# Kernel tuning notes

Measured on AMD Instinct MI355X. Metric: run time of the kernel, lower is better.

## Reference

```python
import jax, jax.numpy as jnp
import numpy as np

H = 8          # query heads
KVH = 1        # key/value heads
HD = 256       # head dim
ROPE_BASE = 10000.0


def _rotate_half(x):
    x1, x2 = x[..., : HD // 2], x[..., HD // 2 :]
    return jnp.concatenate((-x2, x1), axis=-1)


def _rope_cos_sin(position_ids):
    # position_ids: [B, S] int -> cos/sin: [B, S, HD]
    inv_freq = 1.0 / (ROPE_BASE ** (jnp.arange(0, HD, 2, dtype=jnp.float32) / HD))
    freqs = position_ids.astype(jnp.float32)[..., None] * inv_freq  # [B,S,HD/2]
    emb = jnp.concatenate((freqs, freqs), axis=-1)                  # [B,S,HD]
    return jnp.cos(emb), jnp.sin(emb)


def setup_inputs() -> dict:
    key = jax.random.key(0)
    ks = jax.random.split(key, 5)
    B, S, D = 2, 2048, 2048
    return {
        "hidden_states": jax.random.normal(ks[0], (B, S, D), dtype=jnp.float32),
        "attention_mask": jnp.zeros((B, 1, S, S), dtype=jnp.float32),
        "position_ids": jnp.broadcast_to(jnp.arange(S, dtype=jnp.int32), (B, S)),
        "Wq": jax.random.normal(ks[1], (D, H * HD), dtype=jnp.float32) * 0.02,
        "Wk": jax.random.normal(ks[2], (D, KVH * HD), dtype=jnp.float32) * 0.02,
        "Wv": jax.random.normal(ks[3], (D, KVH * HD), dtype=jnp.float32) * 0.02,
        "Wo": jax.random.normal(ks[4], (H * HD, D), dtype=jnp.float32) * 0.02,
    }


def reference(hidden_states, attention_mask, position_ids, Wq, Wk, Wv, Wo):
    B, S, D = hidden_states.shape
    # projections -> [B, heads, S, HD]
    q = jnp.einsum("bsd,df->bsf", hidden_states, Wq).reshape(B, S, H, HD).transpose(0, 2, 1, 3)
    k = jnp.einsum("bsd,df->bsf", hidden_states, Wk).reshape(B, S, KVH, HD).transpose(0, 2, 1, 3)
    v = jnp.einsum("bsd,df->bsf", hidden_states, Wv).reshape(B, S, KVH, HD).transpose(0, 2, 1, 3)

    cos, sin = _rope_cos_sin(position_ids)
    cos, sin = cos[:, None], sin[:, None]  # unsqueeze head dim
    q = q * cos + _rotate_half(q) * sin
    k = k * cos + _rotate_half(k) * sin

    # GQA: repeat kv heads to match query heads
    rep = H // KVH
    k = jnp.repeat(k, rep, axis=1)
    v = jnp.repeat(v, rep, axis=1)

    d_k = D // H  # matches torch code's scaling (== HD here)
    scores = jnp.einsum("bhqd,bhkd->bhqk", q, k) / jnp.sqrt(jnp.float32(d_k))
    scores = scores + attention_mask
    attn = jax.nn.softmax(scores, axis=-1)  # dropout p=0 / eval mode

    out = jnp.einsum("bhqk,bhkd->bhqd", attn, v)  # [B,H,S,HD]
    out = out.transpose(0, 2, 1, 3).reshape(B, S, H * HD)
    out = jnp.einsum("bsf,fd->bsd", out, Wo)
    return out
```

## Files before the change

### kernel.cpp

```cpp
#include <hip/hip_runtime.h>
#include <cmath>


typedef __bf16 bf16;
typedef __attribute__((ext_vector_type(8))) __bf16 bf16x8;
typedef __attribute__((ext_vector_type(4))) __bf16 bf16x4;
typedef __attribute__((ext_vector_type(4))) float f32x4;

#define S_LEN 2048
#define D_MODEL 2048
#define H_NUM 8
#define HDIM 256
#define NT (S_LEN / 64)
#define SM_BIAS 8.0f

#define BAR __builtin_amdgcn_s_barrier()

__device__ __forceinline__ void gl_lds16(const bf16* g, bf16* l) {
  __builtin_amdgcn_global_load_lds(
      (const __attribute__((address_space(1))) void*)g,
      (__attribute__((address_space(3))) void*)l, 16, 0, 0);
}

__global__ void cvt_bf16(const float* __restrict__ src, bf16* __restrict__ dst) {
  const int i = (blockIdx.x * 256 + threadIdx.x) * 4;
  const float4 v = *(const float4*)(src + i);
  bf16x4 o;
  o[0] = (bf16)v.x; o[1] = (bf16)v.y; o[2] = (bf16)v.z; o[3] = (bf16)v.w;
  *(bf16x4*)(dst + i) = o;
}

__global__ void tpose_all(const float* __restrict__ Wq, const float* __restrict__ Wk,
                          const float* __restrict__ Wv, const float* __restrict__ Wo,
                          bf16* __restrict__ Wqkvt, bf16* __restrict__ Wot) {
  __shared__ float t[32][33];
  const int tx = threadIdx.x, ty = threadIdx.y;
  const int bx = blockIdx.x;
  const int k0 = blockIdx.y * 32;
  const float* W; bf16* Wt; int Ncols, no0, n0;
  if (bx < 64)      { W = Wq; Wt = Wqkvt; Ncols = 2048; no0 = 0;    n0 = bx * 32; }
  else if (bx < 72) { W = Wk; Wt = Wqkvt; Ncols = 256;  no0 = 2048; n0 = (bx - 64) * 32; }
  else if (bx < 80) { W = Wv; Wt = Wqkvt; Ncols = 256;  no0 = 2304; n0 = (bx - 72) * 32; }
  else              { W = Wo; Wt = Wot;   Ncols = 2048; no0 = 0;    n0 = (bx - 80) * 32; }
#pragma unroll
  for (int i = 0; i < 4; ++i)
    t[ty + 8 * i][tx] = W[(size_t)(k0 + ty + 8 * i) * Ncols + (n0 + tx)];
  __syncthreads();
#pragma unroll
  for (int i = 0; i < 4; ++i)
    Wt[(size_t)(no0 + n0 + ty + 8 * i) * D_MODEL + (k0 + tx)] = (bf16)t[tx][ty + 8 * i];
}

__global__ __launch_bounds__(512, 2)
void gemm_bf16(const bf16* __restrict__ A, const bf16* __restrict__ Wt,
               bf16* __restrict__ Cq, bf16* __restrict__ Ck, bf16* __restrict__ Cv,
               float* __restrict__ Cf, int NX, int mode) {
  __shared__ bf16 As[2][2][128 * 64];
  __shared__ bf16 Bs[2][2][128 * 64];
  const int tid = threadIdx.x;
  const int lane = tid & 63;
  const int w = tid >> 6;
  const int c16 = lane & 15;
  const int quad = lane >> 4;
  const int wm = w >> 2;
  const int wn = w & 3;

  const int nwg = gridDim.x;
  const int swz = (blockIdx.x & 7) * (nwg >> 3) + (blockIdx.x >> 3);
  const int m0 = (swz / NX) * 256;
  const int n0 = (swz % NX) * 256;

  const char* Ab = (const char*)A;
  const char* Bb = (const char*)Wt;
  const int lr8 = lane >> 3;
  const int scb = ((lane & 7) ^ lr8) << 4;

  f32x4 acc[8][4];
#pragma unroll
  for (int i = 0; i < 8; ++i)
#pragma unroll
    for (int j = 0; j < 4; ++j)
#pragma unroll
      for (int r = 0; r < 4; ++r) acc[i][j][r] = 0.f;

  auto stg = [&](const char* gcol, int grow0, bf16* lhalf) {
#pragma unroll
    for (int j2 = 0; j2 < 2; ++j2) {
      const int c = w * 2 + j2;
      gl_lds16((const bf16*)(gcol + (size_t)(grow0 + c * 8 + lr8) * 4096 + scb),
               lhalf + c * 512);
    }
  };
  auto ldA = [&](int sl, int qm, bf16x8* d) {
    const char* base = (const char*)&As[sl][wm][0];
#pragma unroll
    for (int i = 0; i < 4; ++i) {
      const int row = qm * 64 + i * 16 + c16;
      const int sw = (row & 7) << 4;
#pragma unroll
      for (int kk = 0; kk < 2; ++kk)
        d[i * 2 + kk] = *(const bf16x8*)(base + row * 128 + ((kk * 64 + quad * 16) ^ sw));
    }
  };
  auto ldB = [&](int sl, int qn, bf16x8* d) {
    const char* base = (const char*)&Bs[sl][wn >> 1][0];
#pragma unroll
    for (int j = 0; j < 2; ++j) {
      const int row = (wn & 1) * 64 + qn * 32 + j * 16 + c16;
      const int sw = (row & 7) << 4;
#pragma unroll
      for (int kk = 0; kk < 2; ++kk)
        d[j * 2 + kk] = *(const bf16x8*)(base + row * 128 + ((kk * 64 + quad * 16) ^ sw));
    }
  };
  auto mm = [&](int qm, int qn, const bf16x8* a, const bf16x8* bb) {
    __builtin_amdgcn_s_setprio(1);
#pragma unroll
    for (int kk = 0; kk < 2; ++kk)
#pragma unroll
      for (int i = 0; i < 4; ++i)
#pragma unroll
        for (int j = 0; j < 2; ++j)
          acc[qm * 4 + i][qn * 2 + j] = __builtin_amdgcn_mfma_f32_16x16x32_bf16(
              a[i * 2 + kk], bb[j * 2 + kk], acc[qm * 4 + i][qn * 2 + j], 0, 0, 0);
    __builtin_amdgcn_s_setprio(0);
  };

  bf16x8 Xa[8], Ya[8], Xb[4], Yb[4];

  stg(Ab, m0, &As[0][0][0]);        stg(Ab, m0 + 128, &As[0][1][0]);
  stg(Bb, n0, &Bs[0][0][0]);        stg(Bb, n0 + 128, &Bs[0][1][0]);
  stg(Bb + 128, n0, &Bs[1][0][0]);  stg(Bb + 128, n0 + 128, &Bs[1][1][0]);
  asm volatile("s_waitcnt vmcnt(4)" ::: "memory");
  BAR;

  for (int t = 0; t < 16; ++t) {
    const int kc = t * 256;
    const bool pf = (t < 15);
    ldA(0, 0, Xa); ldB(0, 0, Xb);
    stg(Ab + kc + 128, m0, &As[1][0][0]);
    BAR; mm(0, 0, Xa, Xb); BAR;
    ldB(0, 1, Yb);
    stg(Ab + kc + 128, m0 + 128, &As[1][1][0]);
    BAR; mm(0, 1, Xa, Yb); BAR;
    ldA(0, 1, Ya);
    if (pf) stg(Bb + kc + 256, n0, &Bs[0][0][0]);
    BAR; mm(1, 1, Ya, Yb); BAR;
    if (pf) stg(Bb + kc + 256, n0 + 128, &Bs[0][1][0]);
    BAR; mm(1, 0, Ya, Xb);
    if (pf) asm volatile("s_waitcnt vmcnt(4)" ::: "memory");
    else    asm volatile("s_waitcnt vmcnt(0)" ::: "memory");
    BAR;
    ldA(1, 0, Xa); ldB(1, 0, Xb);
    if (pf) stg(Ab + kc + 256, m0, &As[0][0][0]);
    BAR; mm(0, 0, Xa, Xb); BAR;
    ldB(1, 1, Yb);
    if (pf) stg(Ab + kc + 256, m0 + 128, &As[0][1][0]);
    BAR; mm(0, 1, Xa, Yb); BAR;
    ldA(1, 1, Ya);
    if (pf) stg(Bb + kc + 384, n0, &Bs[1][0][0]);
    BAR; mm(1, 1, Ya, Yb); BAR;
    if (pf) {
      stg(Bb + kc + 384, n0 + 128, &Bs[1][1][0]);
      BAR; mm(1, 0, Ya, Xb);
      asm volatile("s_waitcnt vmcnt(4)" ::: "memory");
      BAR;
    } else {
      BAR; mm(1, 0, Ya, Xb);
    }
  }

#pragma unroll
  for (int i = 0; i < 8; ++i)
#pragma unroll
    for (int j = 0; j < 4; ++j) {
      const int n = n0 + wn * 64 + j * 16 + c16;
#pragma unroll
      for (int r = 0; r < 4; ++r) {
        const int m = m0 + wm * 128 + i * 16 + quad * 4 + r;
        const float val = acc[i][j][r];
        if (mode == 1) {
          const int b = m >> 11, s = m & 2047;
          if (n0 < 2048) {
            const int h = n >> 8, hd = n & 255;
            Cq[((((size_t)b * H_NUM + h) * S_LEN + s) << 8) + hd] = (bf16)val;
          } else if (n0 < 2304) {
            Ck[((size_t)m << 8) + (n - 2048)] = (bf16)val;
          } else {
            Cv[((size_t)((b << 8) + (n - 2304)) << 11) + s] = (bf16)val;
          }
        } else {
          Cf[(size_t)m * D_MODEL + n] = val;
        }
      }
    }
}

#define ROPE_C (-0.07195578415606394f)

__global__ void rope_all(bf16* __restrict__ q, bf16* __restrict__ k,
                         const int* __restrict__ pos, int BHS) {
  const int idx = blockIdx.x * 256 + threadIdx.x;
  const int j = idx & 127;
  const int t = idx >> 7;
  float sn, cs;
  if (t < BHS) {
    const int s = t & 2047;
    const int b = t >> 14;
    const float p = (float)pos[(b << 11) + s];
    sincosf(p * expf((float)j * ROPE_C), &sn, &cs);
    bf16* base = q + ((size_t)t << 8);
    const float x1 = (float)base[j], x2 = (float)base[j + 128];
    base[j] = (bf16)(x1 * cs - x2 * sn);
    base[j + 128] = (bf16)(x2 * cs + x1 * sn);
  } else {
    const int t2 = t - BHS;
    const int s = t2 & 2047;
    const int b = t2 >> 11;
    const float p = (float)pos[(b << 11) + s];
    sincosf(p * expf((float)j * ROPE_C), &sn, &cs);
    bf16* base = k + ((size_t)t2 << 8);
    const float x1 = (float)base[j], x2 = (float)base[j + 128];
    base[j] = (bf16)(x1 * cs - x2 * sn);
    base[j + 128] = (bf16)(x2 * cs + x1 * sn);
  }
}

__global__ __launch_bounds__(512, 2)
void flash_bf16(const bf16* __restrict__ qg, const bf16* __restrict__ kg,
                const bf16* __restrict__ vg, const float* __restrict__ msk,
                bf16* __restrict__ ao) {
  __shared__ bf16 Ks[2][64 * 256];
  __shared__ bf16 Vs[2][256 * 64];
  __shared__ bf16 Ps[128 * 64];
  __shared__ float Lp[2][128];

  const int tid = threadIdx.x;
  const int lane = tid & 63;
  const int w = tid >> 6;
  const int c16 = lane & 15;
  const int quad = lane >> 4;
  const int qi = w & 3;
  const int sec = w >> 2;

  const int bidx = blockIdx.x;
  int b, qb;
  if (gridDim.x == 256) {
    b = (bidx & 7) >> 2;
    qb = ((bidx & 3) << 5) | (bidx >> 3);
  } else {
    b = bidx >> 7;
    qb = bidx & 127;
  }
  const int q0 = qb * 16;

  const bf16* qh = qg + ((((size_t)b * H_NUM + qi * 2) * S_LEN + q0) << 8);
  const char* kbase = (const char*)(kg + ((size_t)b << 19));
  const char* vbase = (const char*)(vg + ((size_t)b << 19));
  const float* mbase = msk + (size_t)b * S_LEN * S_LEN + (size_t)q0 * S_LEN;

  bf16x8 qf[2][8];
#pragma unroll
  for (int mi = 0; mi < 2; ++mi)
#pragma unroll
    for (int kd = 0; kd < 8; ++kd)
      qf[mi][kd] = *(const bf16x8*)&qh[(((size_t)mi * S_LEN + c16) << 8) + kd * 32 + quad * 8];

  f32x4 oacc[2][8];
#pragma unroll
  for (int mi = 0; mi < 2; ++mi)
#pragma unroll
    for (int nj = 0; nj < 8; ++nj)
#pragma unroll
      for (int r = 0; r < 4; ++r) oacc[mi][nj][r] = 0.f;
  float plsum[2][4];
#pragma unroll
  for (int mi = 0; mi < 2; ++mi)
#pragma unroll
    for (int r = 0; r < 4; ++r) plsum[mi][r] = 0.f;

  auto stage = [&](int k0, int buf) {
#pragma unroll
    for (int j = 0; j < 4; ++j) {
      const int ki = w * 4 + j;
      const int krow = ki * 2 + (lane >> 5);
      const int kcb = ((lane & 31) * 16) ^ ((krow & 7) << 4);
      gl_lds16((const bf16*)(kbase + ((size_t)(k0 + krow) << 9) + kcb),
               &Ks[buf][ki * 512]);
      const int vrow = ki * 8 + (lane >> 3);
      const int vcb = ((lane & 7) * 16) ^ ((vrow & 7) << 4);
      gl_lds16((const bf16*)(vbase + ((size_t)vrow << 12) + (k0 << 1) + vcb),
               &Vs[buf][ki * 512]);
    }
  };

  stage(0, 0);
  __syncthreads();

  for (int t = 0; t < NT; ++t) {
    const int k0 = t * 64;
    const int buf = t & 1;
    if (t + 1 < NT) stage(k0 + 64, buf ^ 1);

    float ml[2][4];
#pragma unroll
    for (int nj = 0; nj < 2; ++nj)
#pragma unroll
      for (int r = 0; r < 4; ++r)
        ml[nj][r] = mbase[(size_t)(quad * 4 + r) * S_LEN +
                          k0 + sec * 32 + nj * 16 + c16];

    f32x4 sc[2][2];
#pragma unroll
    for (int mi = 0; mi < 2; ++mi)
#pragma unroll
      for (int nj = 0; nj < 2; ++nj)
#pragma unroll
        for (int r = 0; r < 4; ++r) sc[mi][nj][r] = 0.f;
    __builtin_amdgcn_s_setprio(1);
#pragma unroll
    for (int kd = 0; kd < 8; ++kd) {
      bf16x8 bK[2];
#pragma unroll
      for (int nj = 0; nj < 2; ++nj) {
        const int row = sec * 32 + nj * 16 + c16;
        bK[nj] = *(const bf16x8*)((const char*)&Ks[buf][0] + row * 512 +
                                  ((kd * 64 + quad * 16) ^ ((row & 7) << 4)));
      }
#pragma unroll
      for (int mi = 0; mi < 2; ++mi)
#pragma unroll
        for (int nj = 0; nj < 2; ++nj)
          sc[mi][nj] = __builtin_amdgcn_mfma_f32_16x16x32_bf16(qf[mi][kd], bK[nj], sc[mi][nj], 0, 0, 0);
    }
    __builtin_amdgcn_s_setprio(0);

#pragma unroll
    for (int mi = 0; mi < 2; ++mi)
#pragma unroll
      for (int nj = 0; nj < 2; ++nj)
#pragma unroll
        for (int r = 0; r < 4; ++r) {
          const float p = __expf(sc[mi][nj][r] * 0.0625f + ml[nj][r] - SM_BIAS);
          plsum[mi][r] += p;
          const int row = qi * 32 + mi * 16 + quad * 4 + r;
          const int cb = ((sec * 32 + nj * 16 + c16) * 2) ^ ((row & 7) << 4);
          *(bf16*)((char*)&Ps[0] + row * 128 + cb) = (bf16)p;
        }

    __builtin_amdgcn_sched_barrier(0);
    asm volatile("s_waitcnt lgkmcnt(0)" ::: "memory");
    __builtin_amdgcn_s_barrier();
    __builtin_amdgcn_sched_barrier(0);

    bf16x8 pa[2][2];
#pragma unroll
    for (int mi = 0; mi < 2; ++mi)
#pragma unroll
      for (int ks = 0; ks < 2; ++ks) {
        const int row = qi * 32 + mi * 16 + c16;
        pa[mi][ks] = *(const bf16x8*)((const char*)&Ps[0] + row * 128 +
                                      ((ks * 64 + quad * 16) ^ ((row & 7) << 4)));
      }
    __builtin_amdgcn_s_setprio(1);
#pragma unroll
    for (int nj = 0; nj < 8; ++nj) {
#pragma unroll
      for (int ks = 0; ks < 2; ++ks) {
        const int drow = sec * 128 + nj * 16 + c16;
        const bf16x8 bv = *(const bf16x8*)((const char*)&Vs[buf][0] + drow * 128 +
                                           ((ks * 64 + quad * 16) ^ ((drow & 7) << 4)));
#pragma unroll
        for (int mi = 0; mi < 2; ++mi)
          oacc[mi][nj] = __builtin_amdgcn_mfma_f32_16x16x32_bf16(pa[mi][ks], bv, oacc[mi][nj], 0, 0, 0);
      }
    }
    __builtin_amdgcn_s_setprio(0);

    __syncthreads();
  }

#pragma unroll
  for (int mi = 0; mi < 2; ++mi)
#pragma unroll
    for (int r = 0; r < 4; ++r) {
      float s = plsum[mi][r];
      s += __shfl_xor(s, 1, 64);
      s += __shfl_xor(s, 2, 64);
      s += __shfl_xor(s, 4, 64);
      s += __shfl_xor(s, 8, 64);
      if (c16 == 0) Lp[sec][qi * 32 + mi * 16 + quad * 4 + r] = s;
    }
  __syncthreads();
  float li[2][4];
#pragma unroll
  for (int mi = 0; mi < 2; ++mi)
#pragma unroll
    for (int r = 0; r < 4; ++r) {
      const int row = qi * 32 + mi * 16 + quad * 4 + r;
      li[mi][r] = 1.f / (Lp[0][row] + Lp[1][row]);
    }
  bf16* obase = ao + (size_t)(b * S_LEN + q0 + quad * 4) * D_MODEL + qi * 512 + sec * 128;
#pragma unroll
  for (int mi = 0; mi < 2; ++mi)
#pragma unroll
    for (int nj = 0; nj < 8; ++nj)
#pragma unroll
      for (int r = 0; r < 4; ++r)
        obase[(size_t)r * D_MODEL + mi * 256 + nj * 16 + c16] =
            (bf16)(oacc[mi][nj][r] * li[mi][r]);
}

extern "C" void kernel_launch(void* const* d_in, const int* in_sizes, int n_in,
                              void* d_out, int out_size, void* d_ws, size_t ws_size,
                              hipStream_t stream) {
  const float* hs   = (const float*)d_in[0];
  const float* mask = (const float*)d_in[1];
  const int*   pos  = (const int*)d_in[2];
  const float* Wq   = (const float*)d_in[3];
  const float* Wk   = (const float*)d_in[4];
  const float* Wv   = (const float*)d_in[5];
  const float* Wo   = (const float*)d_in[6];
  float* out = (float*)d_out;

  const int B = in_sizes[2] / S_LEN;
  const int M = B * S_LEN;

  char* wsc = (char*)d_ws;
  bf16* hsb = (bf16*)wsc;
  bf16* aob = hsb;
  size_t off = (size_t)M * D_MODEL * 2;
  bf16* Wqkvt = (bf16*)(wsc + off); off += (size_t)2560 * D_MODEL * 2;
  bf16* Wot   = (bf16*)(wsc + off); off += (size_t)D_MODEL * D_MODEL * 2;
  bf16* kb    = (bf16*)(wsc + off);
  bf16* vb    = kb + (size_t)M * HDIM;

  bf16* qb = (bf16*)d_out;

  const dim3 blk(256);
  cvt_bf16<<<(M * D_MODEL) / 1024, blk, 0, stream>>>(hs, hsb);
  tpose_all<<<dim3(144, 64), dim3(32, 8), 0, stream>>>(Wq, Wk, Wv, Wo, Wqkvt, Wot);

  gemm_bf16<<<10 * (M / 256), dim3(512), 0, stream>>>(hsb, Wqkvt, qb, kb, vb, nullptr, 10, 1);

  rope_all<<<(B * (H_NUM + 1) * S_LEN * 128) / 256, blk, 0, stream>>>(
      qb, kb, pos, B * H_NUM * S_LEN);

  flash_bf16<<<B * (S_LEN / 16), dim3(512), 0, stream>>>(qb, kb, vb, mask, aob);

  gemm_bf16<<<8 * (M / 256), dim3(512), 0, stream>>>(aob, Wot, nullptr, nullptr, nullptr, out, 8, 3);
}
```

Before: 385.8 us.

## Warp-specialize flash attention into QK-softmax and PV producer/consumer groups

Splits the 8 waves of the attention block into two specialized groups. Four waves compute QK^T and the exponentials into a double-buffered P tile, and four waves run the PV MMA on the previous tile, so the two stages overlap across iterations with one barrier per step. K and V staging are also split so K is prefetched one tile ahead while V is loaded for the current tile. Each wave now holds larger register tiles (4x8 output accumulators or 4x8 Q fragments), which raises register pressure under launch_bounds(512,2). The row-sum buffer is aliased onto the K shared buffer to save LDS.

```diff
diff --git a/kernel.cpp b/kernel.cpp
--- a/kernel.cpp
+++ b/kernel.cpp
@@ -232,16 +232,13 @@
                 bf16* __restrict__ ao) {
   __shared__ bf16 Ks[2][64 * 256];
   __shared__ bf16 Vs[2][256 * 64];
-  __shared__ bf16 Ps[128 * 64];
-  __shared__ float Lp[2][128];
+  __shared__ bf16 Ps[2][128 * 64];
 
   const int tid = threadIdx.x;
   const int lane = tid & 63;
   const int w = tid >> 6;
   const int c16 = lane & 15;
   const int quad = lane >> 4;
-  const int qi = w & 3;
-  const int sec = w >> 2;
 
   const int bidx = blockIdx.x;
   int b, qb;
@@ -254,32 +251,11 @@
   }
   const int q0 = qb * 16;
 
-  const bf16* qh = qg + ((((size_t)b * H_NUM + qi * 2) * S_LEN + q0) << 8);
   const char* kbase = (const char*)(kg + ((size_t)b << 19));
   const char* vbase = (const char*)(vg + ((size_t)b << 19));
-  const float* mbase = msk + (size_t)b * S_LEN * S_LEN + (size_t)q0 * S_LEN;
-
-  bf16x8 qf[2][8];
-#pragma unroll
-  for (int mi = 0; mi < 2; ++mi)
-#pragma unroll
-    for (int kd = 0; kd < 8; ++kd)
-      qf[mi][kd] = *(const bf16x8*)&qh[(((size_t)mi * S_LEN + c16) << 8) + kd * 32 + quad * 8];
-
-  f32x4 oacc[2][8];
-#pragma unroll
-  for (int mi = 0; mi < 2; ++mi)
-#pragma unroll
-    for (int nj = 0; nj < 8; ++nj)
-#pragma unroll
-      for (int r = 0; r < 4; ++r) oacc[mi][nj][r] = 0.f;
-  float plsum[2][4];
-#pragma unroll
-  for (int mi = 0; mi < 2; ++mi)
-#pragma unroll
-    for (int r = 0; r < 4; ++r) plsum[mi][r] = 0.f;
-
-  auto stage = [&](int k0, int buf) {
+  float* Lp = (float*)&Ks[0][0];
+
+  auto stage_k = [&](int k0, int buf) {
 #pragma unroll
     for (int j = 0; j < 4; ++j) {
       const int ki = w * 4 + j;
@@ -287,6 +263,12 @@
       const int kcb = ((lane & 31) * 16) ^ ((krow & 7) << 4);
       gl_lds16((const bf16*)(kbase + ((size_t)(k0 + krow) << 9) + kcb),
                &Ks[buf][ki * 512]);
+    }
+  };
+  auto stage_v = [&](int k0, int buf) {
+#pragma unroll
+    for (int j = 0; j < 4; ++j) {
+      const int ki = w * 4 + j;
       const int vrow = ki * 8 + (lane >> 3);
       const int vcb = ((lane & 7) * 16) ^ ((vrow & 7) << 4);
       gl_lds16((const bf16*)(vbase + ((size_t)vrow << 12) + (k0 << 1) + vcb),
@@ -294,121 +276,161 @@
     }
   };
 
-  stage(0, 0);
+  stage_k(0, 0);
   __syncthreads();
 
-  for (int t = 0; t < NT; ++t) {
-    const int k0 = t * 64;
-    const int buf = t & 1;
-    if (t + 1 < NT) stage(k0 + 64, buf ^ 1);
-
-    float ml[2][4];
-#pragma unroll
-    for (int nj = 0; nj < 2; ++nj)
-#pragma unroll
-      for (int r = 0; r < 4; ++r)
-        ml[nj][r] = mbase[(size_t)(quad * 4 + r) * S_LEN +
-                          k0 + sec * 32 + nj * 16 + c16];
-
-    f32x4 sc[2][2];
-#pragma unroll
-    for (int mi = 0; mi < 2; ++mi)
-#pragma unroll
-      for (int nj = 0; nj < 2; ++nj)
-#pragma unroll
-        for (int r = 0; r < 4; ++r) sc[mi][nj][r] = 0.f;
-    __builtin_amdgcn_s_setprio(1);
-#pragma unroll
-    for (int kd = 0; kd < 8; ++kd) {
-      bf16x8 bK[2];
-#pragma unroll
-      for (int nj = 0; nj < 2; ++nj) {
-        const int row = sec * 32 + nj * 16 + c16;
-        bK[nj] = *(const bf16x8*)((const char*)&Ks[buf][0] + row * 512 +
-                                  ((kd * 64 + quad * 16) ^ ((row & 7) << 4)));
+  if (w < 4) {
+    const int mhalf = (w >> 1) & 1;
+    const int khalf = w & 1;
+    const float* mbase = msk + (size_t)b * S_LEN * S_LEN + (size_t)q0 * S_LEN;
+    const bf16* qh = qg + ((((size_t)b * H_NUM + mhalf * 4) * S_LEN + q0) << 8);
+
+    bf16x8 qf[4][8];
+#pragma unroll
+    for (int mi = 0; mi < 4; ++mi)
+#pragma unroll
+      for (int kd = 0; kd < 8; ++kd)
+        qf[mi][kd] = *(const bf16x8*)&qh[(((size_t)mi * S_LEN + c16) << 8) + kd * 32 + quad * 8];
+
+    float plsum[4][4];
+#pragma unroll
+    for (int mi = 0; mi < 4; ++mi)
+#pragma unroll
+      for (int r = 0; r < 4; ++r) plsum[mi][r] = 0.f;
+
+    for (int t = 0; t <= NT; ++t) {
+      if (t + 1 < NT) stage_k((t + 1) * 64, (t + 1) & 1);
+      if (t < NT)     stage_v(t * 64, t & 1);
+      if (t < NT) {
+        const int k0 = t * 64;
+        const int buf = t & 1;
+        float ml[2][4];
+#pragma unroll
+        for (int nj = 0; nj < 2; ++nj)
+#pragma unroll
+          for (int r = 0; r < 4; ++r)
+            ml[nj][r] = mbase[(size_t)(quad * 4 + r) * S_LEN +
+                              k0 + khalf * 32 + nj * 16 + c16];
+
+        f32x4 sc[4][2];
+#pragma unroll
+        for (int mi = 0; mi < 4; ++mi)
+#pragma unroll
+          for (int nj = 0; nj < 2; ++nj)
+#pragma unroll
+            for (int r = 0; r < 4; ++r) sc[mi][nj][r] = 0.f;
+        __builtin_amdgcn_s_setprio(1);
+#pragma unroll
+        for (int kd = 0; kd < 8; ++kd) {
+          bf16x8 bK[2];
+#pragma unroll
+          for (int nj = 0; nj < 2; ++nj) {
+            const int row = khalf * 32 + nj * 16 + c16;
+            bK[nj] = *(const bf16x8*)((const char*)&Ks[buf][0] + row * 512 +
+                                      ((kd * 64 + quad * 16) ^ ((row & 7) << 4)));
+          }
+#pragma unroll
+          for (int mi = 0; mi < 4; ++mi)
+#pragma unroll
+            for (int nj = 0; nj < 2; ++nj)
+              sc[mi][nj] = __builtin_amdgcn_mfma_f32_16x16x32_bf16(qf[mi][kd], bK[nj], sc[mi][nj], 0, 0, 0);
+        }
+        __builtin_amdgcn_s_setprio(0);
+
+        char* pb = (char*)&Ps[t & 1][0];
+#pragma unroll
+        for (int mi = 0; mi < 4; ++mi)
+#pragma unroll
+          for (int nj = 0; nj < 2; ++nj)
+#pragma unroll
+            for (int r = 0; r < 4; ++r) {
+              const float p = __expf(sc[mi][nj][r] * 0.0625f + ml[nj][r] - SM_BIAS);
+              plsum[mi][r] += p;
+              const int row = mhalf * 64 + mi * 16 + quad * 4 + r;
+              const int cb = ((khalf * 32 + nj * 16 + c16) * 2) ^ ((row & 7) << 4);
+              *(bf16*)(pb + row * 128 + cb) = (bf16)p;
+            }
+      } else {
+#pragma unroll
+        for (int mi = 0; mi < 4; ++mi)
+#pragma unroll
+          for (int r = 0; r < 4; ++r) {
+            float s = plsum[mi][r];
+            s += __shfl_xor(s, 1, 64);
+            s += __shfl_xor(s, 2, 64);
+            s += __shfl_xor(s, 4, 64);
+            s += __shfl_xor(s, 8, 64);
+            if (c16 == 0)
+              Lp[khalf * 128 + mhalf * 64 + mi * 16 + quad * 4 + r] = s;
+          }
       }
-#pragma unroll
-      for (int mi = 0; mi < 2; ++mi)
-#pragma unroll
-        for (int nj = 0; nj < 2; ++nj)
-          sc[mi][nj] = __builtin_amdgcn_mfma_f32_16x16x32_bf16(qf[mi][kd], bK[nj], sc[mi][nj], 0, 0, 0);
-    }
-    __builtin_amdgcn_s_setprio(0);
-
-#pragma unroll
-    for (int mi = 0; mi < 2; ++mi)
-#pragma unroll
-      for (int nj = 0; nj < 2; ++nj)
-#pragma unroll
-        for (int r = 0; r < 4; ++r) {
-          const float p = __expf(sc[mi][nj][r] * 0.0625f + ml[nj][r] - SM_BIAS);
-          plsum[mi][r] += p;
-          const int row = qi * 32 + mi * 16 + quad * 4 + r;
-          const int cb = ((sec * 32 + nj * 16 + c16) * 2) ^ ((row & 7) << 4);
-          *(bf16*)((char*)&Ps[0] + row * 128 + cb) = (bf16)p;
+      __syncthreads();
+    }
+  } else {
+    const int pvm = (w >> 1) & 1;
+    const int pvd = w & 1;
+
+    f32x4 oacc[4][8];
+#pragma unroll
+    for (int mi = 0; mi < 4; ++mi)
+#pragma unroll
+      for (int nj = 0; nj < 8; ++nj)
+#pragma unroll
+        for (int r = 0; r < 4; ++r) oacc[mi][nj][r] = 0.f;
+
+    for (int t = 0; t <= NT; ++t) {
+      if (t + 1 < NT) stage_k((t + 1) * 64, (t + 1) & 1);
+      if (t < NT)     stage_v(t * 64, t & 1);
+      if (t > 0) {
+        const int pb = (t - 1) & 1;
+        const char* pbb = (const char*)&Ps[pb][0];
+        const char* vbb = (const char*)&Vs[pb][0];
+        bf16x8 pa[4][2];
+#pragma unroll
+        for (int mi = 0; mi < 4; ++mi)
+#pragma unroll
+          for (int ks = 0; ks < 2; ++ks) {
+            const int row = pvm * 64 + mi * 16 + c16;
+            pa[mi][ks] = *(const bf16x8*)(pbb + row * 128 +
+                                          ((ks * 64 + quad * 16) ^ ((row & 7) << 4)));
+          }
+        __builtin_amdgcn_s_setprio(1);
+#pragma unroll
+        for (int nj = 0; nj < 8; ++nj) {
+#pragma unroll
+          for (int ks = 0; ks < 2; ++ks) {
+            const int drow = pvd * 128 + nj * 16 + c16;
+            const bf16x8 bv = *(const bf16x8*)(vbb + drow * 128 +
+                                               ((ks * 64 + quad * 16) ^ ((drow & 7) << 4)));
+#pragma unroll
+            for (int mi = 0; mi < 4; ++mi)
+              oacc[mi][nj] = __builtin_amdgcn_mfma_f32_16x16x32_bf16(pa[mi][ks], bv, oacc[mi][nj], 0, 0, 0);
+          }
         }
-
-    __builtin_amdgcn_sched_barrier(0);
-    asm volatile("s_waitcnt lgkmcnt(0)" ::: "memory");
-    __builtin_amdgcn_s_barrier();
-    __builtin_amdgcn_sched_barrier(0);
-
-    bf16x8 pa[2][2];
-#pragma unroll
-    for (int mi = 0; mi < 2; ++mi)
-#pragma unroll
-      for (int ks = 0; ks < 2; ++ks) {
-        const int row = qi * 32 + mi * 16 + c16;
-        pa[mi][ks] = *(const bf16x8*)((const char*)&Ps[0] + row * 128 +
-                                      ((ks * 64 + quad * 16) ^ ((row & 7) << 4)));
+        __builtin_amdgcn_s_setprio(0);
       }
-    __builtin_amdgcn_s_setprio(1);
-#pragma unroll
-    for (int nj = 0; nj < 8; ++nj) {
-#pragma unroll
-      for (int ks = 0; ks < 2; ++ks) {
-        const int drow = sec * 128 + nj * 16 + c16;
-        const bf16x8 bv = *(const bf16x8*)((const char*)&Vs[buf][0] + drow * 128 +
-                                           ((ks * 64 + quad * 16) ^ ((drow & 7) << 4)));
-#pragma unroll
-        for (int mi = 0; mi < 2; ++mi)
-          oacc[mi][nj] = __builtin_amdgcn_mfma_f32_16x16x32_bf16(pa[mi][ks], bv, oacc[mi][nj], 0, 0, 0);
+      __syncthreads();
+    }
+
+    float li[4][4];
+#pragma unroll
+    for (int mi = 0; mi < 4; ++mi)
+#pragma unroll
+      for (int r = 0; r < 4; ++r) {
+        const int row = pvm * 64 + mi * 16 + quad * 4 + r;
+        li[mi][r] = 1.f / (Lp[row] + Lp[128 + row]);
       }
-    }
-    __builtin_amdgcn_s_setprio(0);
-
-    __syncthreads();
+    bf16* obase = ao + (size_t)(b * S_LEN + q0 + quad * 4) * D_MODEL +
+                  pvm * 1024 + pvd * 128;
+#pragma unroll
+    for (int mi = 0; mi < 4; ++mi)
+#pragma unroll
+      for (int nj = 0; nj < 8; ++nj)
+#pragma unroll
+        for (int r = 0; r < 4; ++r)
+          obase[(size_t)r * D_MODEL + mi * 256 + nj * 16 + c16] =
+              (bf16)(oacc[mi][nj][r] * li[mi][r]);
   }
-
-#pragma unroll
-  for (int mi = 0; mi < 2; ++mi)
-#pragma unroll
-    for (int r = 0; r < 4; ++r) {
-      float s = plsum[mi][r];
-      s += __shfl_xor(s, 1, 64);
-      s += __shfl_xor(s, 2, 64);
-      s += __shfl_xor(s, 4, 64);
-      s += __shfl_xor(s, 8, 64);
-      if (c16 == 0) Lp[sec][qi * 32 + mi * 16 + quad * 4 + r] = s;
-    }
-  __syncthreads();
-  float li[2][4];
-#pragma unroll
-  for (int mi = 0; mi < 2; ++mi)
-#pragma unroll
-    for (int r = 0; r < 4; ++r) {
-      const int row = qi * 32 + mi * 16 + quad * 4 + r;
-      li[mi][r] = 1.f / (Lp[0][row] + Lp[1][row]);
-    }
-  bf16* obase = ao + (size_t)(b * S_LEN + q0 + quad * 4) * D_MODEL + qi * 512 + sec * 128;
-#pragma unroll
-  for (int mi = 0; mi < 2; ++mi)
-#pragma unroll
-    for (int nj = 0; nj < 8; ++nj)
-#pragma unroll
-      for (int r = 0; r < 4; ++r)
-        obase[(size_t)r * D_MODEL + mi * 256 + nj * 16 + c16] =
-            (bf16)(oacc[mi][nj][r] * li[mi][r]);
 }
 
 extern "C" void kernel_launch(void* const* d_in, const int* in_sizes, int n_in,
```

Measured after the change: 385.8 us. About the same (-0.0%).

## Trim GEMM barriers and restructure attention K/V pipeline with explicit waits

Applied to the files above, without the earlier changes.

In the projection GEMM, the second barrier after each MFMA block is removed and the A-tile prefetch and vmcnt wait are moved earlier, so fewer workgroup barriers fall in the inner loop. In the attention kernel, the loop is unrolled by two with fixed double-buffer indices. Each step issues the next K/V stage and mask load before computing the current tile, and the trailing __syncthreads is replaced by an explicit vmcnt(0) wait plus barrier at the start of each tile. Dropping barriers risks LDS hazards if a buffer is overwritten while other waves are still reading it, and the vmcnt(0) waits may expose load latency.

```diff
diff --git a/kernel.cpp b/kernel.cpp
--- a/kernel.cpp
+++ b/kernel.cpp
@@ -15,6 +15,7 @@
 #define SM_BIAS 8.0f
 
 #define BAR __builtin_amdgcn_s_barrier()
+#define SCHED0 __builtin_amdgcn_sched_barrier(0)
 
 __device__ __forceinline__ void gl_lds16(const bf16* g, bf16* l) {
   __builtin_amdgcn_global_load_lds(
@@ -139,32 +140,33 @@
     const bool pf = (t < 15);
     ldA(0, 0, Xa); ldB(0, 0, Xb);
     stg(Ab + kc + 128, m0, &As[1][0][0]);
-    BAR; mm(0, 0, Xa, Xb); BAR;
+    BAR; mm(0, 0, Xa, Xb);
     ldB(0, 1, Yb);
     stg(Ab + kc + 128, m0 + 128, &As[1][1][0]);
-    BAR; mm(0, 1, Xa, Yb); BAR;
+    BAR; mm(0, 1, Xa, Yb);
     ldA(0, 1, Ya);
     if (pf) stg(Bb + kc + 256, n0, &Bs[0][0][0]);
-    BAR; mm(1, 1, Ya, Yb); BAR;
+    BAR; mm(1, 1, Ya, Yb);
+    if (pf) {
+      stg(Ab + kc + 256, m0, &As[0][0][0]);
+      asm volatile("s_waitcnt vmcnt(4)" ::: "memory");
+    } else {
+      asm volatile("s_waitcnt vmcnt(0)" ::: "memory");
+    }
+    BAR; mm(1, 0, Ya, Xb);
+    ldA(1, 0, Xa); ldB(1, 0, Xb);
     if (pf) stg(Bb + kc + 256, n0 + 128, &Bs[0][1][0]);
-    BAR; mm(1, 0, Ya, Xb);
-    if (pf) asm volatile("s_waitcnt vmcnt(4)" ::: "memory");
-    else    asm volatile("s_waitcnt vmcnt(0)" ::: "memory");
-    BAR;
-    ldA(1, 0, Xa); ldB(1, 0, Xb);
-    if (pf) stg(Ab + kc + 256, m0, &As[0][0][0]);
-    BAR; mm(0, 0, Xa, Xb); BAR;
+    BAR; mm(0, 0, Xa, Xb);
     ldB(1, 1, Yb);
     if (pf) stg(Ab + kc + 256, m0 + 128, &As[0][1][0]);
-    BAR; mm(0, 1, Xa, Yb); BAR;
+    BAR; mm(0, 1, Xa, Yb);
     ldA(1, 1, Ya);
     if (pf) stg(Bb + kc + 384, n0, &Bs[1][0][0]);
-    BAR; mm(1, 1, Ya, Yb); BAR;
+    BAR; mm(1, 1, Ya, Yb);
     if (pf) {
       stg(Bb + kc + 384, n0 + 128, &Bs[1][1][0]);
+      asm volatile("s_waitcnt vmcnt(4)" ::: "memory");
       BAR; mm(1, 0, Ya, Xb);
-      asm volatile("s_waitcnt vmcnt(4)" ::: "memory");
-      BAR;
     } else {
       BAR; mm(1, 0, Ya, Xb);
     }
@@ -279,7 +281,7 @@
 #pragma unroll
     for (int r = 0; r < 4; ++r) plsum[mi][r] = 0.f;
 
-  auto stage = [&](int k0, int buf) {
+  auto stage_kv = [&](int k0, int buf) {
 #pragma unroll
     for (int j = 0; j < 4; ++j) {
       const int ki = w * 4 + j;
@@ -293,23 +295,16 @@
                &Vs[buf][ki * 512]);
     }
   };
-
-  stage(0, 0);
-  __syncthreads();
-
-  for (int t = 0; t < NT; ++t) {
-    const int k0 = t * 64;
-    const int buf = t & 1;
-    if (t + 1 < NT) stage(k0 + 64, buf ^ 1);
-
-    float ml[2][4];
+  auto mask_ld = [&](int k0, float (&ml)[2][4]) {
 #pragma unroll
     for (int nj = 0; nj < 2; ++nj)
 #pragma unroll
       for (int r = 0; r < 4; ++r)
         ml[nj][r] = mbase[(size_t)(quad * 4 + r) * S_LEN +
                           k0 + sec * 32 + nj * 16 + c16];
-
+  };
+
+  auto tile = [&](int k0, int buf, const float (&ml)[2][4]) {
     f32x4 sc[2][2];
 #pragma unroll
     for (int mi = 0; mi < 2; ++mi)
@@ -348,10 +343,10 @@
           *(bf16*)((char*)&Ps[0] + row * 128 + cb) = (bf16)p;
         }
 
-    __builtin_amdgcn_sched_barrier(0);
+    SCHED0;
     asm volatile("s_waitcnt lgkmcnt(0)" ::: "memory");
-    __builtin_amdgcn_s_barrier();
-    __builtin_amdgcn_sched_barrier(0);
+    BAR;
+    SCHED0;
 
     bf16x8 pa[2][2];
 #pragma unroll
@@ -376,8 +371,28 @@
       }
     }
     __builtin_amdgcn_s_setprio(0);
-
-    __syncthreads();
+  };
+
+  float mlA[2][4], mlB[2][4];
+  stage_kv(0, 0);
+  mask_ld(0, mlA);
+
+  for (int u = 0; u < NT / 2; ++u) {
+    const int te = 2 * u;
+    asm volatile("s_waitcnt vmcnt(0)" ::: "memory");
+    BAR;
+    SCHED0;
+    stage_kv((te + 1) * 64, 1);
+    mask_ld((te + 1) * 64, mlB);
+    tile(te * 64, 0, mlA);
+    asm volatile("s_waitcnt vmcnt(0)" ::: "memory");
+    BAR;
+    SCHED0;
+    if (u + 1 < NT / 2) {
+      stage_kv((te + 2) * 64, 0);
+      mask_ld((te + 2) * 64, mlA);
+    }
+    tile((te + 1) * 64, 1, mlB);
   }
 
 #pragma unroll
```

Result: slower. 404.5 us (+4.8%).
